# Kernel optimization log

Measured on AMD Instinct MI355X. Metric: run time of the kernel, lower is better.

## Reference

```python
import jax, jax.numpy as jnp
import numpy as np

EMBED_DIM = 1024
LAMBDA_INIT = 0.8
EPS = 1e-5


def setup_inputs() -> dict:
    key = jax.random.key(0)
    ks = jax.random.split(key, 8)
    D = EMBED_DIM
    x = jax.random.normal(ks[0], (4, 2048, D), dtype=jnp.float32)
    # torch Linear weight [out, in]; we store transposed [in, out] for x @ W
    s = 1.0 / np.sqrt(D)
    w_q12 = jax.random.uniform(ks[1], (D, 2 * D), jnp.float32, -s, s)
    w_k12 = jax.random.uniform(ks[2], (D, 2 * D), jnp.float32, -s, s)
    w_v = jax.random.uniform(ks[3], (D, D), jnp.float32, -s, s)
    lambda_q1 = 0.1 * jax.random.normal(ks[4], (D,), jnp.float32)
    lambda_k1 = 0.1 * jax.random.normal(ks[5], (D,), jnp.float32)
    lambda_q2 = 0.1 * jax.random.normal(ks[6], (D,), jnp.float32)
    lambda_k2 = 0.1 * jax.random.normal(ks[7], (D,), jnp.float32)
    return {"x": x, "w_q12": w_q12, "w_k12": w_k12, "w_v": w_v,
            "lambda_q1": lambda_q1, "lambda_k1": lambda_k1,
            "lambda_q2": lambda_q2, "lambda_k2": lambda_k2}


def reference(x, w_q12, w_k12, w_v, lambda_q1, lambda_k1, lambda_q2, lambda_k2):
    D = x.shape[-1]
    scale = D ** (-0.25)
    q12 = jnp.einsum('bsd,de->bse', x, w_q12)
    k12 = jnp.einsum('bsd,de->bse', x, w_k12)
    q1, q2 = jnp.split(q12, 2, axis=-1)
    k1, k2 = jnp.split(k12, 2, axis=-1)
    v = jnp.einsum('bsd,de->bse', x, w_v)
    attn1 = jnp.einsum('bqd,bkd->bqk', q1, k1) * scale
    attn2 = jnp.einsum('bqd,bkd->bqk', q2, k2) * scale
    lam1 = jnp.exp(jnp.sum(lambda_q1 * lambda_k1))
    lam2 = jnp.exp(jnp.sum(lambda_q2 * lambda_k2))
    lam_full = lam1 - lam2 + LAMBDA_INIT
    diff = jax.nn.softmax(attn1, axis=-1) - lam_full * jax.nn.softmax(attn2, axis=-1)
    out = jnp.einsum('bqk,bkd->bqd', diff, v)
    # RMSNorm (no affine), then scale by (1 - lambda_init)
    rms = jnp.sqrt(jnp.mean(out * out, axis=-1, keepdims=True) + EPS)
    return (out / rms) * (1.0 - LAMBDA_INIT)
```

## Files before the change

### kernel.cpp

```cpp
#include <hip/hip_runtime.h>

typedef float f32x4 __attribute__((ext_vector_type(4)));
typedef _Float16 h16x8 __attribute__((ext_vector_type(8)));
typedef _Float16 h16x4 __attribute__((ext_vector_type(4)));

#define GLOAD_LDS16(gp, lp) __builtin_amdgcn_global_load_lds(               \
    (const __attribute__((address_space(1))) void*)(gp),                    \
    (__attribute__((address_space(3))) void*)(lp), 16, 0, 0)

#define BARX do { __builtin_amdgcn_s_barrier(); asm volatile("" ::: "memory"); } while (0)
#define VMW(N) asm volatile("s_waitcnt vmcnt(" #N ")" ::: "memory")

__global__ __launch_bounds__(256) void cast_x(const float* __restrict__ x,
                                              _Float16* __restrict__ xh) {
  long i = (long)blockIdx.x * 256 + threadIdx.x;
  f32x4 a = *(const f32x4*)(x + i * 8);
  f32x4 b = *(const f32x4*)(x + i * 8 + 4);
  h16x8 h;
  h[0] = (_Float16)a[0]; h[1] = (_Float16)a[1];
  h[2] = (_Float16)a[2]; h[3] = (_Float16)a[3];
  h[4] = (_Float16)b[0]; h[5] = (_Float16)b[1];
  h[6] = (_Float16)b[2]; h[7] = (_Float16)b[3];
  *(h16x8*)(xh + i * 8) = h;
}

__global__ __launch_bounds__(256) void tcw(const float* __restrict__ in,
                                           _Float16* __restrict__ out,
                                           int Kd, int Nd, float scale) {
  __shared__ float tile[64][65];
  const int t = threadIdx.x;
  const int k0 = blockIdx.y * 64, n0 = blockIdx.x * 64;
  const int tr = t >> 4, tc = (t & 15) * 4;
#pragma unroll
  for (int i = 0; i < 4; ++i) {
    int r = i * 16 + tr;
    f32x4 a = *(const f32x4*)(in + (long)(k0 + r) * Nd + n0 + tc);
    tile[r][tc + 0] = a[0]; tile[r][tc + 1] = a[1];
    tile[r][tc + 2] = a[2]; tile[r][tc + 3] = a[3];
  }
  __syncthreads();
#pragma unroll
  for (int i = 0; i < 4; ++i) {
    int r = i * 16 + tr;
    h16x4 h;
#pragma unroll
    for (int q = 0; q < 4; ++q) h[q] = (_Float16)(tile[tc + q][r] * scale);
    *(h16x4*)(out + (long)(n0 + r) * Kd + k0 + tc) = h;
  }
}

__global__ __launch_bounds__(256) void trans16(const _Float16* __restrict__ in,
                                               _Float16* __restrict__ out,
                                               int R, int Cd, long ibatch, long obatch) {
  __shared__ _Float16 tile[64][72];
  in += (long)blockIdx.z * ibatch;
  out += (long)blockIdx.z * obatch;
  const int t = threadIdx.x;
  const int r0 = blockIdx.y * 64, c0 = blockIdx.x * 64;
  const int tr = t >> 3, tc8 = (t & 7) * 8;
#pragma unroll
  for (int i = 0; i < 2; ++i) {
    int r = i * 32 + tr;
    h16x8 a = *(const h16x8*)(in + (long)(r0 + r) * Cd + c0 + tc8);
    *(h16x8*)(&tile[r][tc8]) = a;
  }
  __syncthreads();
#pragma unroll
  for (int i = 0; i < 2; ++i) {
    int r = i * 32 + tr;
    h16x8 h;
#pragma unroll
    for (int q = 0; q < 8; ++q) h[q] = tile[tc8 + q][r];
    *(h16x8*)(out + (long)(c0 + r) * R + r0 + tc8) = h;
  }
}

__global__ __launch_bounds__(1024) void lambda_k(const float* __restrict__ lq1,
                                                 const float* __restrict__ lk1,
                                                 const float* __restrict__ lq2,
                                                 const float* __restrict__ lk2,
                                                 float* __restrict__ lam) {
  __shared__ float sh1[16], sh2[16];
  const int t = threadIdx.x;
  float p1 = lq1[t] * lk1[t];
  float p2 = lq2[t] * lk2[t];
#pragma unroll
  for (int off = 1; off < 64; off <<= 1) {
    p1 += __shfl_xor(p1, off);
    p2 += __shfl_xor(p2, off);
  }
  if ((t & 63) == 0) { sh1[t >> 6] = p1; sh2[t >> 6] = p2; }
  __syncthreads();
  if (t == 0) {
    float s1 = 0.f, s2 = 0.f;
    for (int i = 0; i < 16; ++i) { s1 += sh1[i]; s2 += sh2[i]; }
    lam[0] = __expf(s1) - __expf(s2) + 0.8f;
  }
}

template <int MW, int NW, typename CT>
__global__ __launch_bounds__(MW * NW * 64, 4) void gemmw(
    const _Float16* __restrict__ A, const _Float16* __restrict__ B,
    CT* __restrict__ C, int K, int lda, int ldb, int ldc,
    long abatch, long bbatch, long cbatch, long a2, long c2, int natt,
    int nbx, int nby) {
  constexpr int BM = MW * 64, BN = NW * 64;
  constexpr int THREADS = MW * NW * 64;
  constexpr int nA = BM * 4 / THREADS;
  constexpr int nB = BN * 4 / THREADS;
  constexpr int L = nA + nB;
  __shared__ _Float16 As[3][BM][32];
  __shared__ _Float16 Bs[3][BN][32];

  const int nwg = gridDim.x;
  const int orig = blockIdx.x;
  const int qd = nwg >> 3, rm = nwg & 7;
  const int xcd = orig & 7, sub = orig >> 3;
  const int wgid = (xcd < rm ? xcd * (qd + 1) : rm * (qd + 1) + (xcd - rm) * qd) + sub;

  const int z = wgid / (nbx * nby);
  const int rem = wgid - z * nbx * nby;
  const int by = rem / nbx;
  const int bx = rem - by * nbx;
  const int att = z % natt;
  const int bz = z / natt;

  const int t = threadIdx.x;
  const int lane = t & 63, wv = t >> 6;
  const int wm = wv >> 1, wn = wv & 1;
  const int lg = lane >> 4, l15 = lane & 15;

  const _Float16* Ab = A + (long)bz * abatch + (long)att * a2 + (long)(by * BM) * lda;
  const _Float16* Bb = B + (long)bz * bbatch + (long)att * a2 + (long)(bx * BN) * ldb;

  auto stage = [&](int slot, int S) {
    const long ko = (long)S * 32;
#pragma unroll
    for (int j = 0; j < nA; ++j) {
      const int e = t + j * THREADS;
      const int r = e >> 2;
      const int gs = ((e & 3) - (r >> 1)) & 3;
      GLOAD_LDS16(Ab + (long)r * lda + ko + gs * 8, &As[slot][0][0] + e * 8);
    }
#pragma unroll
    for (int j = 0; j < nB; ++j) {
      const int e = t + j * THREADS;
      const int r = e >> 2;
      const int gs = ((e & 3) - (r >> 1)) & 3;
      GLOAD_LDS16(Bb + (long)r * ldb + ko + gs * 8, &Bs[slot][0][0] + e * 8);
    }
  };

  int offA[4], offB[4];
#pragma unroll
  for (int m = 0; m < 4; ++m) {
    const int r = wm * 64 + m * 16 + l15;
    offA[m] = (r * 4 + ((lg + (r >> 1)) & 3)) * 8;
  }
#pragma unroll
  for (int n = 0; n < 4; ++n) {
    const int r = wn * 64 + n * 16 + l15;
    offB[n] = (r * 4 + ((lg + (r >> 1)) & 3)) * 8;
  }

  f32x4 acc[4][4] = {};
  const int NS = K >> 5;

  stage(0, 0); stage(1, 1);
  int cur = 0, nx2 = 2;

  for (int S = 0; S < NS; ++S) {
    if (S == NS - 1) VMW(0);
    else { if constexpr (L == 3) VMW(3); else VMW(4); }
    BARX;

    if (S + 2 < NS) stage(nx2, S + 2);

    const _Float16* Ap = &As[cur][0][0];
    const _Float16* Bp = &Bs[cur][0][0];
    h16x8 a[4], b[4];
#pragma unroll
    for (int m = 0; m < 4; ++m) a[m] = *(const h16x8*)(Ap + offA[m]);
#pragma unroll
    for (int n = 0; n < 4; ++n) b[n] = *(const h16x8*)(Bp + offB[n]);
    __builtin_amdgcn_s_setprio(1);
#pragma unroll
    for (int m = 0; m < 4; ++m)
#pragma unroll
      for (int n = 0; n < 4; ++n)
        acc[m][n] = __builtin_amdgcn_mfma_f32_16x16x32_f16(a[m], b[n], acc[m][n], 0, 0, 0);
    __builtin_amdgcn_s_setprio(0);

    cur = (cur == 2) ? 0 : cur + 1;
    nx2 = (nx2 == 2) ? 0 : nx2 + 1;
  }

  CT* Cb = C + (long)bz * cbatch + (long)att * c2;
  const int crow0 = by * BM + wm * 64;
  const int ccol0 = bx * BN + wn * 64;
#pragma unroll
  for (int m = 0; m < 4; ++m)
#pragma unroll
    for (int n = 0; n < 4; ++n)
#pragma unroll
      for (int j = 0; j < 4; ++j)
        Cb[(long)(crow0 + m * 16 + lg * 4 + j) * ldc + ccol0 + n * 16 + l15] =
            (CT)acc[m][n][j];
}

__global__ __launch_bounds__(256) void softmax_diff(const _Float16* __restrict__ S1,
                                                    const _Float16* __restrict__ S2,
                                                    _Float16* __restrict__ D,
                                                    const float* __restrict__ lamp) {
  const long row = (long)blockIdx.x * 4 + (threadIdx.x >> 6);
  const int lane = threadIdx.x & 63;
  const float lam = *lamp;
  const _Float16* s1 = S1 + row * 2048;
  const _Float16* s2 = S2 + row * 2048;
  float v1[32], v2[32];
  float m1 = -3e38f, m2 = -3e38f;
#pragma unroll
  for (int j = 0; j < 4; ++j) {
    h16x8 a = ((const h16x8*)s1)[j * 64 + lane];
    h16x8 b = ((const h16x8*)s2)[j * 64 + lane];
#pragma unroll
    for (int q = 0; q < 8; ++q) {
      v1[j * 8 + q] = (float)a[q]; v2[j * 8 + q] = (float)b[q];
      m1 = fmaxf(m1, v1[j * 8 + q]); m2 = fmaxf(m2, v2[j * 8 + q]);
    }
  }
#pragma unroll
  for (int off = 1; off < 64; off <<= 1) {
    m1 = fmaxf(m1, __shfl_xor(m1, off));
    m2 = fmaxf(m2, __shfl_xor(m2, off));
  }
  float l1 = 0.f, l2 = 0.f;
#pragma unroll
  for (int e = 0; e < 32; ++e) {
    v1[e] = __expf(v1[e] - m1); l1 += v1[e];
    v2[e] = __expf(v2[e] - m2); l2 += v2[e];
  }
#pragma unroll
  for (int off = 1; off < 64; off <<= 1) {
    l1 += __shfl_xor(l1, off);
    l2 += __shfl_xor(l2, off);
  }
  const float r1 = 1.f / l1, r2 = lam / l2;
  _Float16* d = D + row * 2048;
#pragma unroll
  for (int j = 0; j < 4; ++j) {
    h16x8 h;
#pragma unroll
    for (int q = 0; q < 8; ++q)
      h[q] = (_Float16)(v1[j * 8 + q] * r1 - v2[j * 8 + q] * r2);
    ((h16x8*)d)[j * 64 + lane] = h;
  }
}

__global__ __launch_bounds__(256) void rmsnorm(const _Float16* __restrict__ O,
                                               float* __restrict__ out) {
  const long row = (long)blockIdx.x * 4 + (threadIdx.x >> 6);
  const int lane = threadIdx.x & 63;
  const _Float16* o = O + row * 1024;
  h16x8 a = ((const h16x8*)o)[lane];
  h16x8 b = ((const h16x8*)o)[64 + lane];
  float xa[8], xb[8];
  float ss = 0.f;
#pragma unroll
  for (int q = 0; q < 8; ++q) {
    xa[q] = (float)a[q]; xb[q] = (float)b[q];
    ss += xa[q] * xa[q] + xb[q] * xb[q];
  }
#pragma unroll
  for (int off = 1; off < 64; off <<= 1) ss += __shfl_xor(ss, off);
  const float s = 0.2f * rsqrtf(ss * (1.f / 1024.f) + 1e-5f);
  float* po = out + row * 1024;
  f32x4 r;
#pragma unroll
  for (int q = 0; q < 4; ++q) r[q] = xa[q] * s;
  *(f32x4*)(po + lane * 8) = r;
#pragma unroll
  for (int q = 0; q < 4; ++q) r[q] = xa[4 + q] * s;
  *(f32x4*)(po + lane * 8 + 4) = r;
#pragma unroll
  for (int q = 0; q < 4; ++q) r[q] = xb[q] * s;
  *(f32x4*)(po + 512 + lane * 8) = r;
#pragma unroll
  for (int q = 0; q < 4; ++q) r[q] = xb[4 + q] * s;
  *(f32x4*)(po + 512 + lane * 8 + 4) = r;
}

extern "C" void kernel_launch(void* const* d_in, const int* in_sizes, int n_in,
                              void* d_out, int out_size, void* d_ws, size_t ws_size,
                              hipStream_t stream) {
  const float* x   = (const float*)d_in[0];
  const float* wq  = (const float*)d_in[1];
  const float* wk  = (const float*)d_in[2];
  const float* wv  = (const float*)d_in[3];
  const float* lq1 = (const float*)d_in[4];
  const float* lk1 = (const float*)d_in[5];
  const float* lq2 = (const float*)d_in[6];
  const float* lk2 = (const float*)d_in[7];
  float* out = (float*)d_out;

  const size_t MB = 1ull << 20;
  char* ws = (char*)d_ws;
  _Float16* xh   = (_Float16*)(ws + 0);
  _Float16* Wp   = (_Float16*)(ws + 16 * MB);
  _Float16* qkv  = (_Float16*)(ws + 26 * MB);
  _Float16* vt   = (_Float16*)(ws + 106 * MB);
  _Float16* S1   = (_Float16*)(ws + 122 * MB);
  _Float16* S2   = (_Float16*)(ws + 154 * MB);
  float*    lam  = (float*)(ws + 186 * MB);
  _Float16* diff = (_Float16*)(ws + 26 * MB);
  _Float16* opre = (_Float16*)(ws + 58 * MB);

  const float scale = 0.17677669529663689f;

  cast_x<<<4096, 256, 0, stream>>>(x, xh);
  tcw<<<dim3(32, 16), 256, 0, stream>>>(wq, Wp, 1024, 2048, scale);
  tcw<<<dim3(32, 16), 256, 0, stream>>>(wk, Wp + 2048l * 1024, 1024, 2048, 1.0f);
  tcw<<<dim3(16, 16), 256, 0, stream>>>(wv, Wp + 4096l * 1024, 1024, 1024, 1.0f);
  lambda_k<<<1, 1024, 0, stream>>>(lq1, lk1, lq2, lk2, lam);

  gemmw<4, 2, _Float16><<<1280, 512, 0, stream>>>(xh, Wp, qkv, 1024, 1024, 1024, 5120,
                                                  0, 0, 0, 0, 0, 1, 40, 32);

  trans16<<<dim3(16, 32, 4), 256, 0, stream>>>(qkv + 4096, vt, 2048, 5120,
                                               2048l * 5120, 1024l * 2048);

  gemmw<4, 2, _Float16><<<1024, 512, 0, stream>>>(qkv, qkv + 2048, S1, 1024, 5120, 5120, 2048,
                                                  2048l * 5120, 2048l * 5120, 2048l * 2048,
                                                  1024, 16777216l, 2, 16, 8);

  softmax_diff<<<2048, 256, 0, stream>>>(S1, S2, diff, lam);

  gemmw<2, 2, _Float16><<<512, 256, 0, stream>>>(diff, vt, opre, 2048, 2048, 2048, 1024,
                                                 2048l * 2048, 1024l * 2048, 2048l * 1024,
                                                 0, 0, 1, 8, 16);

  rmsnorm<<<2048, 256, 0, stream>>>(opre, out);
}
```

Before: 286.6 us.

## Pre-swizzle operands into MFMA fragment layout and load GEMM tiles directly to registers

Producers (cast, weight transpose, QKV epilogue, softmax) now write fp16 data already arranged in per-lane MFMA fragment order. The GEMMs can then load A and B straight from global memory into registers, with no LDS staging and no barriers in the main loop. The V transpose kernel is folded into the QKV GEMM epilogue, and each wave computes a larger 128x64 tile using register double buffering. The trade-off is more pressure on L2 and HBM, since tiles are no longer shared through LDS across waves. It also loses the latency hiding that the async global-to-LDS pipeline provided, and the larger accumulator raises register usage.

```diff
diff --git a/kernel.cpp b/kernel.cpp
--- a/kernel.cpp
+++ b/kernel.cpp
@@ -2,77 +2,39 @@
 
 typedef float f32x4 __attribute__((ext_vector_type(4)));
 typedef _Float16 h16x8 __attribute__((ext_vector_type(8)));
-typedef _Float16 h16x4 __attribute__((ext_vector_type(4)));
-
-#define GLOAD_LDS16(gp, lp) __builtin_amdgcn_global_load_lds(               \
-    (const __attribute__((address_space(1))) void*)(gp),                    \
-    (__attribute__((address_space(3))) void*)(lp), 16, 0, 0)
-
-#define BARX do { __builtin_amdgcn_s_barrier(); asm volatile("" ::: "memory"); } while (0)
-#define VMW(N) asm volatile("s_waitcnt vmcnt(" #N ")" ::: "memory")
-
-__global__ __launch_bounds__(256) void cast_x(const float* __restrict__ x,
-                                              _Float16* __restrict__ xh) {
-  long i = (long)blockIdx.x * 256 + threadIdx.x;
-  f32x4 a = *(const f32x4*)(x + i * 8);
-  f32x4 b = *(const f32x4*)(x + i * 8 + 4);
+
+#define LGKM0 asm volatile("s_waitcnt lgkmcnt(0)" ::: "memory")
+
+
+__global__ __launch_bounds__(256) void cast_xn(const float* __restrict__ x,
+                                               h16x8* __restrict__ xhN) {
+  const int w = blockIdx.x * 4 + (threadIdx.x >> 6);
+  const int lane = threadIdx.x & 63;
+  const int l15 = lane & 15, lg = lane >> 4;
+  const int rb = w >> 5, kc = w & 31;
+  const float* src = x + (long)(rb * 16 + l15) * 1024 + kc * 32 + lg * 8;
+  f32x4 a = *(const f32x4*)src;
+  f32x4 b = *(const f32x4*)(src + 4);
   h16x8 h;
   h[0] = (_Float16)a[0]; h[1] = (_Float16)a[1];
   h[2] = (_Float16)a[2]; h[3] = (_Float16)a[3];
   h[4] = (_Float16)b[0]; h[5] = (_Float16)b[1];
   h[6] = (_Float16)b[2]; h[7] = (_Float16)b[3];
-  *(h16x8*)(xh + i * 8) = h;
-}
-
-__global__ __launch_bounds__(256) void tcw(const float* __restrict__ in,
-                                           _Float16* __restrict__ out,
-                                           int Kd, int Nd, float scale) {
-  __shared__ float tile[64][65];
-  const int t = threadIdx.x;
-  const int k0 = blockIdx.y * 64, n0 = blockIdx.x * 64;
-  const int tr = t >> 4, tc = (t & 15) * 4;
-#pragma unroll
-  for (int i = 0; i < 4; ++i) {
-    int r = i * 16 + tr;
-    f32x4 a = *(const f32x4*)(in + (long)(k0 + r) * Nd + n0 + tc);
-    tile[r][tc + 0] = a[0]; tile[r][tc + 1] = a[1];
-    tile[r][tc + 2] = a[2]; tile[r][tc + 3] = a[3];
-  }
-  __syncthreads();
-#pragma unroll
-  for (int i = 0; i < 4; ++i) {
-    int r = i * 16 + tr;
-    h16x4 h;
-#pragma unroll
-    for (int q = 0; q < 4; ++q) h[q] = (_Float16)(tile[tc + q][r] * scale);
-    *(h16x4*)(out + (long)(n0 + r) * Kd + k0 + tc) = h;
-  }
-}
-
-__global__ __launch_bounds__(256) void trans16(const _Float16* __restrict__ in,
-                                               _Float16* __restrict__ out,
-                                               int R, int Cd, long ibatch, long obatch) {
-  __shared__ _Float16 tile[64][72];
-  in += (long)blockIdx.z * ibatch;
-  out += (long)blockIdx.z * obatch;
-  const int t = threadIdx.x;
-  const int r0 = blockIdx.y * 64, c0 = blockIdx.x * 64;
-  const int tr = t >> 3, tc8 = (t & 7) * 8;
-#pragma unroll
-  for (int i = 0; i < 2; ++i) {
-    int r = i * 32 + tr;
-    h16x8 a = *(const h16x8*)(in + (long)(r0 + r) * Cd + c0 + tc8);
-    *(h16x8*)(&tile[r][tc8]) = a;
-  }
-  __syncthreads();
-#pragma unroll
-  for (int i = 0; i < 2; ++i) {
-    int r = i * 32 + tr;
-    h16x8 h;
-#pragma unroll
-    for (int q = 0; q < 8; ++q) h[q] = tile[tc8 + q][r];
-    *(h16x8*)(out + (long)(c0 + r) * R + r0 + tc8) = h;
-  }
+  xhN[(long)w * 64 + lane] = h;
+}
+
+__global__ __launch_bounds__(256) void tcwn(const float* __restrict__ W,
+                                            h16x8* __restrict__ WpN,
+                                            int Nd, int nofs, float scale) {
+  const int w = blockIdx.x * 4 + (threadIdx.x >> 6);
+  const int lane = threadIdx.x & 63;
+  const int l15 = lane & 15, lg = lane >> 4;
+  const int nb = w >> 5, kc = w & 31;
+  const float* src = W + (long)(kc * 32 + lg * 8) * Nd + nb * 16 + l15;
+  h16x8 h;
+#pragma unroll
+  for (int i = 0; i < 8; ++i) h[i] = (_Float16)(src[(long)i * Nd] * scale);
+  WpN[((long)(nofs + nb) * 32 + kc) * 64 + lane] = h;
 }
 
 __global__ __launch_bounds__(1024) void lambda_k(const float* __restrict__ lq1,
@@ -98,162 +60,211 @@
   }
 }
 
-template <int MW, int NW, typename CT>
-__global__ __launch_bounds__(MW * NW * 64, 4) void gemmw(
-    const _Float16* __restrict__ A, const _Float16* __restrict__ B,
-    CT* __restrict__ C, int K, int lda, int ldb, int ldc,
-    long abatch, long bbatch, long cbatch, long a2, long c2, int natt,
-    int nbx, int nby) {
-  constexpr int BM = MW * 64, BN = NW * 64;
-  constexpr int THREADS = MW * NW * 64;
-  constexpr int nA = BM * 4 / THREADS;
-  constexpr int nB = BN * 4 / THREADS;
-  constexpr int L = nA + nB;
-  __shared__ _Float16 As[3][BM][32];
-  __shared__ _Float16 Bs[3][BN][32];
-
-  const int nwg = gridDim.x;
-  const int orig = blockIdx.x;
-  const int qd = nwg >> 3, rm = nwg & 7;
-  const int xcd = orig & 7, sub = orig >> 3;
-  const int wgid = (xcd < rm ? xcd * (qd + 1) : rm * (qd + 1) + (xcd - rm) * qd) + sub;
-
-  const int z = wgid / (nbx * nby);
-  const int rem = wgid - z * nbx * nby;
-  const int by = rem / nbx;
-  const int bx = rem - by * nbx;
-  const int att = z % natt;
-  const int bz = z / natt;
-
-  const int t = threadIdx.x;
-  const int lane = t & 63, wv = t >> 6;
+template <int MODE>
+__global__ __launch_bounds__(256, 2) void gemmf(
+    const h16x8* __restrict__ A0, const h16x8* __restrict__ B0,
+    _Float16* __restrict__ out0, h16x8* __restrict__ outN,
+    h16x8* __restrict__ vtN) {
+  constexpr int NS = (MODE == 2) ? 64 : 32;
+  constexpr int CS = (MODE == 0) ? 32 : (MODE == 1) ? 128 : 64;
+
+  const int nwg = gridDim.x, orig = blockIdx.x;
+  const int wgid = (orig & 7) * (nwg >> 3) + (orig >> 3);
+
+  int bm, bn, z = 0, att = 0;
+  if constexpr (MODE == 0) { bm = wgid & 31; bn = wgid >> 5; }
+  else if constexpr (MODE == 1) {
+    const int b = wgid >> 7, r = wgid & 127;
+    bm = r & 7; bn = r >> 3; att = b >> 2; z = b & 3;
+  } else { bm = wgid & 31; bn = wgid >> 5; }
+
+  const int t = threadIdx.x, lane = t & 63, wv = t >> 6;
   const int wm = wv >> 1, wn = wv & 1;
-  const int lg = lane >> 4, l15 = lane & 15;
-
-  const _Float16* Ab = A + (long)bz * abatch + (long)att * a2 + (long)(by * BM) * lda;
-  const _Float16* Bb = B + (long)bz * bbatch + (long)att * a2 + (long)(bx * BN) * ldb;
-
-  auto stage = [&](int slot, int S) {
-    const long ko = (long)S * 32;
-#pragma unroll
-    for (int j = 0; j < nA; ++j) {
-      const int e = t + j * THREADS;
-      const int r = e >> 2;
-      const int gs = ((e & 3) - (r >> 1)) & 3;
-      GLOAD_LDS16(Ab + (long)r * lda + ko + gs * 8, &As[slot][0][0] + e * 8);
-    }
-#pragma unroll
-    for (int j = 0; j < nB; ++j) {
-      const int e = t + j * THREADS;
-      const int r = e >> 2;
-      const int gs = ((e & 3) - (r >> 1)) & 3;
-      GLOAD_LDS16(Bb + (long)r * ldb + ko + gs * 8, &Bs[slot][0][0] + e * 8);
-    }
+  const int l15 = lane & 15, lg = lane >> 4;
+  const int mt = bm * 2 + wm, nt = bn * 2 + wn;
+
+  long Ac, Bc;
+  if constexpr (MODE == 0) {
+    Ac = (long)mt * 8 * 32;
+    Bc = (long)nt * 4 * 32;
+  } else if constexpr (MODE == 1) {
+    Ac = ((long)z * 128 + mt * 8) * 128 + att * 32;
+    Bc = ((long)z * 128 + nt * 4) * 128 + 64 + att * 32;
+  } else {
+    const int zz = mt >> 4;
+    Ac = ((long)zz * 128 + (mt & 15) * 8) * 64;
+    Bc = ((long)zz * 64 + nt * 4) * 64;
+  }
+  const h16x8* Aw = A0 + Ac * 64 + lane;
+  const h16x8* Bw = B0 + Bc * 64 + lane;
+
+  f32x4 acc[8][4] = {};
+  h16x8 aE[8], aO[8], bE[4], bO[4];
+
+  auto lda = [&](h16x8(&d)[8], int kc) {
+#pragma unroll
+    for (int m = 0; m < 8; ++m) d[m] = Aw[((long)m * CS + kc) * 64];
   };
-
-  int offA[4], offB[4];
-#pragma unroll
-  for (int m = 0; m < 4; ++m) {
-    const int r = wm * 64 + m * 16 + l15;
-    offA[m] = (r * 4 + ((lg + (r >> 1)) & 3)) * 8;
-  }
-#pragma unroll
-  for (int n = 0; n < 4; ++n) {
-    const int r = wn * 64 + n * 16 + l15;
-    offB[n] = (r * 4 + ((lg + (r >> 1)) & 3)) * 8;
-  }
-
-  f32x4 acc[4][4] = {};
-  const int NS = K >> 5;
-
-  stage(0, 0); stage(1, 1);
-  int cur = 0, nx2 = 2;
-
-  for (int S = 0; S < NS; ++S) {
-    if (S == NS - 1) VMW(0);
-    else { if constexpr (L == 3) VMW(3); else VMW(4); }
-    BARX;
-
-    if (S + 2 < NS) stage(nx2, S + 2);
-
-    const _Float16* Ap = &As[cur][0][0];
-    const _Float16* Bp = &Bs[cur][0][0];
-    h16x8 a[4], b[4];
-#pragma unroll
-    for (int m = 0; m < 4; ++m) a[m] = *(const h16x8*)(Ap + offA[m]);
-#pragma unroll
-    for (int n = 0; n < 4; ++n) b[n] = *(const h16x8*)(Bp + offB[n]);
-    __builtin_amdgcn_s_setprio(1);
-#pragma unroll
-    for (int m = 0; m < 4; ++m)
+  auto ldb = [&](h16x8(&d)[4], int kc) {
+#pragma unroll
+    for (int n = 0; n < 4; ++n) d[n] = Bw[((long)n * CS + kc) * 64];
+  };
+  auto step = [&](h16x8(&a)[8], h16x8(&b)[4]) {
+#pragma unroll
+    for (int m = 0; m < 8; ++m)
 #pragma unroll
       for (int n = 0; n < 4; ++n)
         acc[m][n] = __builtin_amdgcn_mfma_f32_16x16x32_f16(a[m], b[n], acc[m][n], 0, 0, 0);
-    __builtin_amdgcn_s_setprio(0);
-
-    cur = (cur == 2) ? 0 : cur + 1;
-    nx2 = (nx2 == 2) ? 0 : nx2 + 1;
-  }
-
-  CT* Cb = C + (long)bz * cbatch + (long)att * c2;
-  const int crow0 = by * BM + wm * 64;
-  const int ccol0 = bx * BN + wn * 64;
-#pragma unroll
-  for (int m = 0; m < 4; ++m)
-#pragma unroll
-    for (int n = 0; n < 4; ++n)
-#pragma unroll
-      for (int j = 0; j < 4; ++j)
-        Cb[(long)(crow0 + m * 16 + lg * 4 + j) * ldc + ccol0 + n * 16 + l15] =
-            (CT)acc[m][n][j];
-}
-
-__global__ __launch_bounds__(256) void softmax_diff(const _Float16* __restrict__ S1,
-                                                    const _Float16* __restrict__ S2,
-                                                    _Float16* __restrict__ D,
-                                                    const float* __restrict__ lamp) {
-  const long row = (long)blockIdx.x * 4 + (threadIdx.x >> 6);
-  const int lane = threadIdx.x & 63;
+  };
+
+  lda(aE, 0); ldb(bE, 0);
+  lda(aO, 1); ldb(bO, 1);
+#pragma unroll 1
+  for (int kc = 0; kc < NS; kc += 2) {
+    step(aE, bE);
+    lda(aE, kc + 2); ldb(bE, kc + 2);
+    step(aO, bO);
+    lda(aO, kc + 3); ldb(bO, kc + 3);
+  }
+
+  __shared__ float smem[4][2048];
+  float* sw = smem[wv];
+
+  if constexpr (MODE == 0) {
+    if (nt < 64) {
+#pragma unroll
+      for (int m = 0; m < 8; ++m) {
+        LGKM0;
+#pragma unroll
+        for (int n = 0; n < 4; ++n)
+          *(f32x4*)(sw + (n * 16 + l15) * 16 + lg * 4) = acc[m][n];
+        LGKM0;
+#pragma unroll
+        for (int h = 0; h < 2; ++h) {
+          h16x8 hv;
+#pragma unroll
+          for (int i = 0; i < 8; ++i)
+            hv[i] = (_Float16)sw[(h * 32 + lg * 8 + i) * 16 + l15];
+          outN[(((long)mt * 8 + m) * 128 + nt * 2 + h) * 64 + lane] = hv;
+        }
+      }
+    } else {
+      const int ntv = nt - 64;
+      const int zz = mt >> 4, mtl = mt & 15;
+      h16x8* vz = vtN + (long)zz * 4096 * 64;
+#pragma unroll
+      for (int p = 0; p < 4; ++p) {
+        LGKM0;
+#pragma unroll
+        for (int qq = 0; qq < 2; ++qq)
+#pragma unroll
+          for (int n = 0; n < 4; ++n)
+            *(f32x4*)(sw + (n * 16 + l15) * 32 + qq * 16 + lg * 4) = acc[p * 2 + qq][n];
+        LGKM0;
+#pragma unroll
+        for (int d = 0; d < 4; ++d) {
+          f32x4 lo = *(const f32x4*)(sw + (d * 16 + l15) * 32 + lg * 8);
+          f32x4 hi = *(const f32x4*)(sw + (d * 16 + l15) * 32 + lg * 8 + 4);
+          h16x8 hv;
+          hv[0] = (_Float16)lo[0]; hv[1] = (_Float16)lo[1];
+          hv[2] = (_Float16)lo[2]; hv[3] = (_Float16)lo[3];
+          hv[4] = (_Float16)hi[0]; hv[5] = (_Float16)hi[1];
+          hv[6] = (_Float16)hi[2]; hv[7] = (_Float16)hi[3];
+          vz[(((long)ntv * 4 + d) * 64 + mtl * 4 + p) * 64 + lane] = hv;
+        }
+      }
+    }
+  } else {
+    _Float16* orow;
+    long ldc;
+    if constexpr (MODE == 1) {
+      orow = out0 + ((long)att * 4 + z) * 2048 * 2048 + (long)mt * 128 * 2048 + nt * 64;
+      ldc = 2048;
+    } else {
+      orow = out0 + (long)mt * 128 * 1024 + nt * 64;
+      ldc = 1024;
+    }
+#pragma unroll
+    for (int m = 0; m < 8; ++m) {
+      LGKM0;
+#pragma unroll
+      for (int n = 0; n < 4; ++n)
+        *(f32x4*)(sw + (n * 16 + l15) * 16 + lg * 4) = acc[m][n];
+      LGKM0;
+#pragma unroll
+      for (int h = 0; h < 2; ++h) {
+        const int rl = h * 8 + (lane >> 3), c8 = lane & 7;
+        h16x8 hv;
+#pragma unroll
+        for (int i = 0; i < 8; ++i)
+          hv[i] = (_Float16)sw[(c8 * 8 + i) * 16 + rl];
+        *(h16x8*)(orow + (long)(m * 16 + rl) * ldc + c8 * 8) = hv;
+      }
+    }
+  }
+}
+
+__global__ __launch_bounds__(256) void softmax_diffn(
+    const _Float16* __restrict__ Sb, h16x8* __restrict__ diffN,
+    const float* __restrict__ lamp) {
+  __shared__ _Float16 dl[16][2056];
+  const int rb = blockIdx.x;
+  const int z = rb >> 7, rbl = rb & 127;
+  const int t = threadIdx.x, lane = t & 63, wv = t >> 6;
+  const int l15 = lane & 15, lg = lane >> 4;
   const float lam = *lamp;
-  const _Float16* s1 = S1 + row * 2048;
-  const _Float16* s2 = S2 + row * 2048;
-  float v1[32], v2[32];
-  float m1 = -3e38f, m2 = -3e38f;
-#pragma unroll
-  for (int j = 0; j < 4; ++j) {
-    h16x8 a = ((const h16x8*)s1)[j * 64 + lane];
-    h16x8 b = ((const h16x8*)s2)[j * 64 + lane];
-#pragma unroll
-    for (int q = 0; q < 8; ++q) {
-      v1[j * 8 + q] = (float)a[q]; v2[j * 8 + q] = (float)b[q];
-      m1 = fmaxf(m1, v1[j * 8 + q]); m2 = fmaxf(m2, v2[j * 8 + q]);
-    }
-  }
-#pragma unroll
-  for (int off = 1; off < 64; off <<= 1) {
-    m1 = fmaxf(m1, __shfl_xor(m1, off));
-    m2 = fmaxf(m2, __shfl_xor(m2, off));
-  }
-  float l1 = 0.f, l2 = 0.f;
-#pragma unroll
-  for (int e = 0; e < 32; ++e) {
-    v1[e] = __expf(v1[e] - m1); l1 += v1[e];
-    v2[e] = __expf(v2[e] - m2); l2 += v2[e];
-  }
-#pragma unroll
-  for (int off = 1; off < 64; off <<= 1) {
-    l1 += __shfl_xor(l1, off);
-    l2 += __shfl_xor(l2, off);
-  }
-  const float r1 = 1.f / l1, r2 = lam / l2;
-  _Float16* d = D + row * 2048;
-#pragma unroll
-  for (int j = 0; j < 4; ++j) {
-    h16x8 h;
-#pragma unroll
-    for (int q = 0; q < 8; ++q)
-      h[q] = (_Float16)(v1[j * 8 + q] * r1 - v2[j * 8 + q] * r2);
-    ((h16x8*)d)[j * 64 + lane] = h;
+  const _Float16* S1r = Sb + (long)z * 2048 * 2048 + (long)rbl * 16 * 2048;
+  const _Float16* S2r = S1r + (long)4 * 2048 * 2048;
+
+  for (int qi = 0; qi < 4; ++qi) {
+    const int r = wv * 4 + qi;
+    const _Float16* s1 = S1r + (long)r * 2048;
+    const _Float16* s2 = S2r + (long)r * 2048;
+    float v1[32], v2[32];
+    float m1 = -3e38f, m2 = -3e38f;
+#pragma unroll
+    for (int j = 0; j < 4; ++j) {
+      h16x8 a = ((const h16x8*)s1)[j * 64 + lane];
+      h16x8 b = ((const h16x8*)s2)[j * 64 + lane];
+#pragma unroll
+      for (int q = 0; q < 8; ++q) {
+        v1[j * 8 + q] = (float)a[q]; v2[j * 8 + q] = (float)b[q];
+        m1 = fmaxf(m1, v1[j * 8 + q]); m2 = fmaxf(m2, v2[j * 8 + q]);
+      }
+    }
+#pragma unroll
+    for (int off = 1; off < 64; off <<= 1) {
+      m1 = fmaxf(m1, __shfl_xor(m1, off));
+      m2 = fmaxf(m2, __shfl_xor(m2, off));
+    }
+    float l1 = 0.f, l2 = 0.f;
+#pragma unroll
+    for (int e = 0; e < 32; ++e) {
+      v1[e] = __expf(v1[e] - m1); l1 += v1[e];
+      v2[e] = __expf(v2[e] - m2); l2 += v2[e];
+    }
+#pragma unroll
+    for (int off = 1; off < 64; off <<= 1) {
+      l1 += __shfl_xor(l1, off);
+      l2 += __shfl_xor(l2, off);
+    }
+    const float r1 = 1.f / l1, r2 = lam / l2;
+#pragma unroll
+    for (int j = 0; j < 4; ++j) {
+      h16x8 h;
+#pragma unroll
+      for (int q = 0; q < 8; ++q)
+        h[q] = (_Float16)(v1[j * 8 + q] * r1 - v2[j * 8 + q] * r2);
+      *(h16x8*)(&dl[r][(j * 64 + lane) * 8]) = h;
+    }
+  }
+  __syncthreads();
+  h16x8* dz = diffN + (long)z * 8192 * 64;
+#pragma unroll
+  for (int cc = 0; cc < 16; ++cc) {
+    const int kc = wv * 16 + cc;
+    h16x8 hv = *(const h16x8*)(&dl[l15][kc * 32 + lg * 8]);
+    dz[((long)rbl * 64 + kc) * 64 + lane] = hv;
   }
 }
 
@@ -305,39 +316,30 @@
 
   const size_t MB = 1ull << 20;
   char* ws = (char*)d_ws;
-  _Float16* xh   = (_Float16*)(ws + 0);
-  _Float16* Wp   = (_Float16*)(ws + 16 * MB);
-  _Float16* qkv  = (_Float16*)(ws + 26 * MB);
-  _Float16* vt   = (_Float16*)(ws + 106 * MB);
-  _Float16* S1   = (_Float16*)(ws + 122 * MB);
-  _Float16* S2   = (_Float16*)(ws + 154 * MB);
-  float*    lam  = (float*)(ws + 186 * MB);
-  _Float16* diff = (_Float16*)(ws + 26 * MB);
-  _Float16* opre = (_Float16*)(ws + 58 * MB);
+  h16x8*    xhN   = (h16x8*)(ws + 0);
+  h16x8*    WpN   = (h16x8*)(ws + 16 * MB);
+  h16x8*    qkvN  = (h16x8*)(ws + 26 * MB);
+  h16x8*    vtN   = (h16x8*)(ws + 90 * MB);
+  _Float16* Sbuf  = (_Float16*)(ws + 106 * MB);
+  h16x8*    diffN = (h16x8*)(ws + 170 * MB);
+  _Float16* opre  = (_Float16*)(ws + 202 * MB);
+  float*    lam   = (float*)(ws + 218 * MB);
 
   const float scale = 0.17677669529663689f;
 
-  cast_x<<<4096, 256, 0, stream>>>(x, xh);
-  tcw<<<dim3(32, 16), 256, 0, stream>>>(wq, Wp, 1024, 2048, scale);
-  tcw<<<dim3(32, 16), 256, 0, stream>>>(wk, Wp + 2048l * 1024, 1024, 2048, 1.0f);
-  tcw<<<dim3(16, 16), 256, 0, stream>>>(wv, Wp + 4096l * 1024, 1024, 1024, 1.0f);
+  cast_xn<<<4096, 256, 0, stream>>>(x, xhN);
+  tcwn<<<1024, 256, 0, stream>>>(wq, WpN, 2048, 0, scale);
+  tcwn<<<1024, 256, 0, stream>>>(wk, WpN, 2048, 128, 1.0f);
+  tcwn<<<512, 256, 0, stream>>>(wv, WpN, 1024, 256, 1.0f);
   lambda_k<<<1, 1024, 0, stream>>>(lq1, lk1, lq2, lk2, lam);
 
-  gemmw<4, 2, _Float16><<<1280, 512, 0, stream>>>(xh, Wp, qkv, 1024, 1024, 1024, 5120,
-                                                  0, 0, 0, 0, 0, 1, 40, 32);
-
-  trans16<<<dim3(16, 32, 4), 256, 0, stream>>>(qkv + 4096, vt, 2048, 5120,
-                                               2048l * 5120, 1024l * 2048);
-
-  gemmw<4, 2, _Float16><<<1024, 512, 0, stream>>>(qkv, qkv + 2048, S1, 1024, 5120, 5120, 2048,
-                                                  2048l * 5120, 2048l * 5120, 2048l * 2048,
-                                                  1024, 16777216l, 2, 16, 8);
-
-  softmax_diff<<<2048, 256, 0, stream>>>(S1, S2, diff, lam);
-
-  gemmw<2, 2, _Float16><<<512, 256, 0, stream>>>(diff, vt, opre, 2048, 2048, 2048, 1024,
-                                                 2048l * 2048, 1024l * 2048, 2048l * 1024,
-                                                 0, 0, 1, 8, 16);
+  gemmf<0><<<1280, 256, 0, stream>>>(xhN, WpN, nullptr, qkvN, vtN);
+
+  gemmf<1><<<1024, 256, 0, stream>>>(qkvN, qkvN, Sbuf, nullptr, nullptr);
+
+  softmax_diffn<<<512, 256, 0, stream>>>(Sbuf, diffN, lam);
+
+  gemmf<2><<<256, 256, 0, stream>>>(diffN, vtN, opre, nullptr, nullptr);
 
   rmsnorm<<<2048, 256, 0, stream>>>(opre, out);
 }
```

New measurement: 299.1 us. +4.4%, slower.

## Switch GEMMs to 32x32x16 MFMA with 256x128 tiles and XOR swizzle

Applied to the files above, without the earlier changes.

Replaces the templated 16x16x32 MFMA GEMM with a single 4-wave kernel that uses 32x32x16 MFMA instructions. Each wave computes a 128x64 sub-tile, so the block tile becomes 256x128. The LDS layout changes to an XOR swizzle. The larger tile per wave raises operand reuse from LDS and cuts the number of MFMA issues. In exchange it needs more accumulator registers (occupancy bound set to 2 blocks) and launches fewer blocks, notably only 256 for the final PV GEMM, which may underfill the GPU.

```diff
diff --git a/kernel.cpp b/kernel.cpp
--- a/kernel.cpp
+++ b/kernel.cpp
@@ -1,6 +1,7 @@
 #include <hip/hip_runtime.h>
 
 typedef float f32x4 __attribute__((ext_vector_type(4)));
+typedef float f32x16 __attribute__((ext_vector_type(16)));
 typedef _Float16 h16x8 __attribute__((ext_vector_type(8)));
 typedef _Float16 h16x4 __attribute__((ext_vector_type(4)));
 
@@ -98,19 +99,14 @@
   }
 }
 
-template <int MW, int NW, typename CT>
-__global__ __launch_bounds__(MW * NW * 64, 4) void gemmw(
+template <typename CT>
+__global__ __launch_bounds__(256, 2) void gemmx(
     const _Float16* __restrict__ A, const _Float16* __restrict__ B,
     CT* __restrict__ C, int K, int lda, int ldb, int ldc,
     long abatch, long bbatch, long cbatch, long a2, long c2, int natt,
     int nbx, int nby) {
-  constexpr int BM = MW * 64, BN = NW * 64;
-  constexpr int THREADS = MW * NW * 64;
-  constexpr int nA = BM * 4 / THREADS;
-  constexpr int nB = BN * 4 / THREADS;
-  constexpr int L = nA + nB;
-  __shared__ _Float16 As[3][BM][32];
-  __shared__ _Float16 Bs[3][BN][32];
+  __shared__ _Float16 As[3][256 * 32];
+  __shared__ _Float16 Bs[3][128 * 32];
 
   const int nwg = gridDim.x;
   const int orig = blockIdx.x;
@@ -128,42 +124,39 @@
   const int t = threadIdx.x;
   const int lane = t & 63, wv = t >> 6;
   const int wm = wv >> 1, wn = wv & 1;
-  const int lg = lane >> 4, l15 = lane & 15;
-
-  const _Float16* Ab = A + (long)bz * abatch + (long)att * a2 + (long)(by * BM) * lda;
-  const _Float16* Bb = B + (long)bz * bbatch + (long)att * a2 + (long)(bx * BN) * ldb;
+  const int l31 = lane & 31, lh = lane >> 5;
+
+  const _Float16* Ab = A + (long)bz * abatch + (long)att * a2 + (long)(by * 256) * lda;
+  const _Float16* Bb = B + (long)bz * bbatch + (long)att * a2 + (long)(bx * 128) * ldb;
 
   auto stage = [&](int slot, int S) {
     const long ko = (long)S * 32;
 #pragma unroll
-    for (int j = 0; j < nA; ++j) {
-      const int e = t + j * THREADS;
+    for (int j = 0; j < 4; ++j) {
+      const int e = t + j * 256;
       const int r = e >> 2;
-      const int gs = ((e & 3) - (r >> 1)) & 3;
-      GLOAD_LDS16(Ab + (long)r * lda + ko + gs * 8, &As[slot][0][0] + e * 8);
-    }
-#pragma unroll
-    for (int j = 0; j < nB; ++j) {
-      const int e = t + j * THREADS;
+      const int gs = (e & 3) ^ (r & 3);
+      GLOAD_LDS16(Ab + (long)r * lda + ko + gs * 8, &As[slot][e * 8]);
+    }
+#pragma unroll
+    for (int j = 0; j < 2; ++j) {
+      const int e = t + j * 256;
       const int r = e >> 2;
-      const int gs = ((e & 3) - (r >> 1)) & 3;
-      GLOAD_LDS16(Bb + (long)r * ldb + ko + gs * 8, &Bs[slot][0][0] + e * 8);
+      const int gs = (e & 3) ^ (r & 3);
+      GLOAD_LDS16(Bb + (long)r * ldb + ko + gs * 8, &Bs[slot][e * 8]);
     }
   };
 
-  int offA[4], offB[4];
-#pragma unroll
-  for (int m = 0; m < 4; ++m) {
-    const int r = wm * 64 + m * 16 + l15;
-    offA[m] = (r * 4 + ((lg + (r >> 1)) & 3)) * 8;
-  }
-#pragma unroll
-  for (int n = 0; n < 4; ++n) {
-    const int r = wn * 64 + n * 16 + l15;
-    offB[n] = (r * 4 + ((lg + (r >> 1)) & 3)) * 8;
-  }
-
-  f32x4 acc[4][4] = {};
+  int swz[2];
+#pragma unroll
+  for (int kh = 0; kh < 2; ++kh) swz[kh] = ((kh * 2 + lh) ^ (lane & 3)) * 8;
+  int offA[4], offB[2];
+#pragma unroll
+  for (int mf = 0; mf < 4; ++mf) offA[mf] = (wm * 128 + mf * 32 + l31) * 32;
+#pragma unroll
+  for (int nf = 0; nf < 2; ++nf) offB[nf] = (wn * 64 + nf * 32 + l31) * 32;
+
+  f32x16 acc[4][2] = {};
   const int NS = K >> 5;
 
   stage(0, 0); stage(1, 1);
@@ -171,24 +164,32 @@
 
   for (int S = 0; S < NS; ++S) {
     if (S == NS - 1) VMW(0);
-    else { if constexpr (L == 3) VMW(3); else VMW(4); }
+    else VMW(6);
     BARX;
 
     if (S + 2 < NS) stage(nx2, S + 2);
 
-    const _Float16* Ap = &As[cur][0][0];
-    const _Float16* Bp = &Bs[cur][0][0];
-    h16x8 a[4], b[4];
-#pragma unroll
-    for (int m = 0; m < 4; ++m) a[m] = *(const h16x8*)(Ap + offA[m]);
-#pragma unroll
-    for (int n = 0; n < 4; ++n) b[n] = *(const h16x8*)(Bp + offB[n]);
+    const _Float16* Ap = &As[cur][0];
+    const _Float16* Bp = &Bs[cur][0];
+    h16x8 a0[4], a1[4], b0[2], b1[2];
+#pragma unroll
+    for (int mf = 0; mf < 4; ++mf) {
+      a0[mf] = *(const h16x8*)(Ap + offA[mf] + swz[0]);
+      a1[mf] = *(const h16x8*)(Ap + offA[mf] + swz[1]);
+    }
+#pragma unroll
+    for (int nf = 0; nf < 2; ++nf) {
+      b0[nf] = *(const h16x8*)(Bp + offB[nf] + swz[0]);
+      b1[nf] = *(const h16x8*)(Bp + offB[nf] + swz[1]);
+    }
     __builtin_amdgcn_s_setprio(1);
 #pragma unroll
-    for (int m = 0; m < 4; ++m)
-#pragma unroll
-      for (int n = 0; n < 4; ++n)
-        acc[m][n] = __builtin_amdgcn_mfma_f32_16x16x32_f16(a[m], b[n], acc[m][n], 0, 0, 0);
+    for (int mf = 0; mf < 4; ++mf)
+#pragma unroll
+      for (int nf = 0; nf < 2; ++nf) {
+        acc[mf][nf] = __builtin_amdgcn_mfma_f32_32x32x16_f16(a0[mf], b0[nf], acc[mf][nf], 0, 0, 0);
+        acc[mf][nf] = __builtin_amdgcn_mfma_f32_32x32x16_f16(a1[mf], b1[nf], acc[mf][nf], 0, 0, 0);
+      }
     __builtin_amdgcn_s_setprio(0);
 
     cur = (cur == 2) ? 0 : cur + 1;
@@ -196,16 +197,18 @@
   }
 
   CT* Cb = C + (long)bz * cbatch + (long)att * c2;
-  const int crow0 = by * BM + wm * 64;
-  const int ccol0 = bx * BN + wn * 64;
-#pragma unroll
-  for (int m = 0; m < 4; ++m)
-#pragma unroll
-    for (int n = 0; n < 4; ++n)
-#pragma unroll
-      for (int j = 0; j < 4; ++j)
-        Cb[(long)(crow0 + m * 16 + lg * 4 + j) * ldc + ccol0 + n * 16 + l15] =
-            (CT)acc[m][n][j];
+  const int crow0 = by * 256 + wm * 128;
+  const int ccol0 = bx * 128 + wn * 64;
+#pragma unroll
+  for (int mf = 0; mf < 4; ++mf)
+#pragma unroll
+    for (int nf = 0; nf < 2; ++nf)
+#pragma unroll
+      for (int reg = 0; reg < 16; ++reg) {
+        const int row = crow0 + mf * 32 + (reg & 3) + 8 * (reg >> 2) + 4 * lh;
+        const int col = ccol0 + nf * 32 + l31;
+        Cb[(long)row * ldc + col] = (CT)acc[mf][nf][reg];
+      }
 }
 
 __global__ __launch_bounds__(256) void softmax_diff(const _Float16* __restrict__ S1,
@@ -323,21 +326,21 @@
   tcw<<<dim3(16, 16), 256, 0, stream>>>(wv, Wp + 4096l * 1024, 1024, 1024, 1.0f);
   lambda_k<<<1, 1024, 0, stream>>>(lq1, lk1, lq2, lk2, lam);
 
-  gemmw<4, 2, _Float16><<<1280, 512, 0, stream>>>(xh, Wp, qkv, 1024, 1024, 1024, 5120,
-                                                  0, 0, 0, 0, 0, 1, 40, 32);
+  gemmx<_Float16><<<1280, 256, 0, stream>>>(xh, Wp, qkv, 1024, 1024, 1024, 5120,
+                                            0, 0, 0, 0, 0, 1, 40, 32);
 
   trans16<<<dim3(16, 32, 4), 256, 0, stream>>>(qkv + 4096, vt, 2048, 5120,
                                                2048l * 5120, 1024l * 2048);
 
-  gemmw<4, 2, _Float16><<<1024, 512, 0, stream>>>(qkv, qkv + 2048, S1, 1024, 5120, 5120, 2048,
-                                                  2048l * 5120, 2048l * 5120, 2048l * 2048,
-                                                  1024, 16777216l, 2, 16, 8);
+  gemmx<_Float16><<<1024, 256, 0, stream>>>(qkv, qkv + 2048, S1, 1024, 5120, 5120, 2048,
+                                            2048l * 5120, 2048l * 5120, 2048l * 2048,
+                                            1024, 16777216l, 2, 16, 8);
 
   softmax_diff<<<2048, 256, 0, stream>>>(S1, S2, diff, lam);
 
-  gemmw<2, 2, _Float16><<<512, 256, 0, stream>>>(diff, vt, opre, 2048, 2048, 2048, 1024,
-                                                 2048l * 2048, 1024l * 2048, 2048l * 1024,
-                                                 0, 0, 1, 8, 16);
+  gemmx<_Float16><<<256, 256, 0, stream>>>(diff, vt, opre, 2048, 2048, 2048, 1024,
+                                           2048l * 2048, 1024l * 2048, 2048l * 1024,
+                                           0, 0, 1, 8, 8);
 
   rmsnorm<<<2048, 256, 0, stream>>>(opre, out);
 }
```

Result: slower. 367.0 us (+28.1%).
